# Optimization experiments

Measured on AMD Instinct MI355X. Metric: run time of the kernel, lower is better.

## Reference

```python
import jax, jax.numpy as jnp
import numpy as np

TOP_K = 8
TEMPERATURE = 0.07
EPS = 1e-12  # matches torch F.normalize eps


def l2norm(x):
    return x / jnp.maximum(jnp.linalg.norm(x, axis=-1, keepdims=True), EPS)


def setup_inputs() -> dict:
    key = jax.random.key(0)
    k1, k2, k3, k4 = jax.random.split(key, 4)
    B, D, V, U, Q = 256, 768, 50257, 1000, 10000
    time_series_embedding = jax.random.normal(k1, (B, D), dtype=jnp.float32)
    word_embeddings = jax.random.normal(k2, (V, D), dtype=jnp.float32)
    # xavier_uniform-like init scale for the prototype parameter
    limit = float(np.sqrt(6.0 / (U + D)))
    tctp_embeddings = jax.random.uniform(k3, (U, D), dtype=jnp.float32, minval=-limit, maxval=limit)
    support_set = jax.random.normal(k4, (Q, D), dtype=jnp.float32)
    return {
        "time_series_embedding": time_series_embedding,
        "word_embeddings": word_embeddings,
        "tctp_embeddings": tctp_embeddings,
        "support_set": support_set,
    }


def reference(time_series_embedding, word_embeddings, tctp_embeddings, support_set):
    B = time_series_embedding.shape[0]

    # ---- L_proto: MSE between each word token and its nearest prototype ----
    # For unit vectors, cdist^2 = 2 - 2*cos_sim, so argmin(dist) == argmax(sim).
    w_norm = l2norm(word_embeddings)          # [V, D]
    t_norm = l2norm(tctp_embeddings)          # [U, D]
    sim_vu = jnp.einsum('vd,ud->vu', w_norm, t_norm)  # [V, U]
    nearest_idx = jnp.argmax(sim_vu, axis=1)          # [V]
    nearest_protos = t_norm[nearest_idx]              # [V, D]
    loss_proto = jnp.mean((w_norm - nearest_protos) ** 2)

    # ---- top-k nearest-neighbor TCTPs from the support set ----
    ts_norm = l2norm(time_series_embedding)   # [B, D]
    sup_norm = l2norm(support_set)            # [Q, D]
    sim_bq = jnp.einsum('bd,qd->bq', ts_norm, sup_norm)  # [B, Q]
    # smallest L2 distance == largest cosine similarity (unit vectors)
    _, topk_idx = jax.lax.top_k(sim_bq, TOP_K)           # [B, k]
    nearest_tctps = sup_norm[topk_idx]                   # [B, k, D]

    # ---- NNCL contrastive loss ----
    positive = l2norm(nearest_tctps.mean(axis=1))        # [B, D]
    pos_sim = jnp.sum(ts_norm * positive, axis=1) / TEMPERATURE   # [B]
    neg_sim = jnp.einsum('bd,cd->bc', ts_norm, ts_norm) / TEMPERATURE  # [B, B]
    neg_sim = jnp.where(jnp.eye(B, dtype=bool), -jnp.inf, neg_sim)
    logits = jnp.concatenate([pos_sim[:, None], neg_sim], axis=1)  # [B, 1+B]
    loss_nncl = -jnp.mean(jax.nn.log_softmax(logits, axis=1)[:, 0])

    return nearest_tctps, loss_proto, loss_nncl
```

## Files before the change

### kernel.cpp

```cpp
#include <hip/hip_runtime.h>
#include <hip/hip_bf16.h>
#include <math.h>

typedef __bf16 bf16_t;
typedef __bf16 bf16x8 __attribute__((ext_vector_type(8)));
typedef __bf16 bf16x4 __attribute__((ext_vector_type(4)));
typedef float  f32x4  __attribute__((ext_vector_type(4)));
typedef long   i64_t;
typedef unsigned long long u64_t;

#define D 768

__device__ inline double blk_sum(double x, double* s) {
#pragma unroll
  for (int m = 32; m; m >>= 1) x += __shfl_xor(x, m);
  __syncthreads();
  if ((threadIdx.x & 63) == 0) s[threadIdx.x >> 6] = x;
  __syncthreads();
  return s[0] + s[1] + s[2] + s[3];
}

__device__ inline double blk_max(double x, double* s) {
#pragma unroll
  for (int m = 32; m; m >>= 1) x = fmax(x, __shfl_xor(x, m));
  __syncthreads();
  if ((threadIdx.x & 63) == 0) s[threadIdx.x >> 6] = x;
  __syncthreads();
  return fmax(fmax(s[0], s[1]), fmax(s[2], s[3]));
}

__global__ __launch_bounds__(256) void norm_all(
    const float* __restrict__ Tm, const float* __restrict__ TS,
    const float* __restrict__ SUP, const float* __restrict__ Wm,
    u64_t* __restrict__ t8T, u64_t* __restrict__ w8t,
    float* __restrict__ wscale, float* __restrict__ ts_n,
    bf16_t* __restrict__ ts_bf, float* __restrict__ sup_n,
    double* __restrict__ accd,
    int U, int V, int B, int Q, int nbT, int nbTS, int nbSUP) {
  const int wave = threadIdx.x >> 6, lane = threadIdx.x & 63;
  const int bid = blockIdx.x;
  if (bid == 0 && threadIdx.x == 0) accd[0] = 0.0;

  if (bid < nbT) {
    const int row = bid * 4 + wave;
    double inv = 0.0;
    if (row < U) {
      const float4* s = (const float4*)(Tm + (size_t)row * D);
      double ss = 0.0;
#pragma unroll
      for (int j = 0; j < 3; j++) {
        float4 v = s[lane + 64 * j];
        ss += (double)v.x * v.x + (double)v.y * v.y +
              (double)v.z * v.z + (double)v.w * v.w;
      }
#pragma unroll
      for (int m = 32; m; m >>= 1) ss += __shfl_xor(ss, m);
      inv = 1.0 / fmax(sqrt(ss), 1e-12);
    }
    const float sc = (float)(inv * 16.0);
#pragma unroll
    for (int h = 0; h < 2; h++) {
      if (h == 1 && lane >= 32) continue;
      const int c = h * 64 + lane;
      u64_t frag = 0ull;
      if (row < U) {
        const float* p = Tm + (size_t)row * D + c * 8;
        float4 x = *(const float4*)p;
        float4 y = *(const float4*)(p + 4);
        int lo = __builtin_amdgcn_cvt_pk_fp8_f32(x.x * sc, x.y * sc, 0, false);
        lo = __builtin_amdgcn_cvt_pk_fp8_f32(x.z * sc, x.w * sc, lo, true);
        int hi = __builtin_amdgcn_cvt_pk_fp8_f32(y.x * sc, y.y * sc, 0, false);
        hi = __builtin_amdgcn_cvt_pk_fp8_f32(y.z * sc, y.w * sc, hi, true);
        frag = ((u64_t)(unsigned)hi << 32) | (unsigned)lo;
      }
      t8T[(size_t)c * 1024 + row] = frag;
    }
    return;
  }

  if (bid < nbT + nbTS + nbSUP) {
    const float* src;
    int row;
    bool is_ts = false;
    if (bid < nbT + nbTS) { row = (bid - nbT) * 4 + wave; src = TS; is_ts = true; }
    else                  { row = (bid - nbT - nbTS) * 4 + wave; src = SUP;
                            if (row >= Q) return; }
    const float4* s = (const float4*)(src + (size_t)row * D);
    float4 v[3];
    double ss = 0.0;
#pragma unroll
    for (int j = 0; j < 3; j++) {
      v[j] = s[lane + 64 * j];
      ss += (double)v[j].x * v[j].x + (double)v[j].y * v[j].y +
            (double)v[j].z * v[j].z + (double)v[j].w * v[j].w;
    }
#pragma unroll
    for (int m = 32; m; m >>= 1) ss += __shfl_xor(ss, m);
    double inv = 1.0 / fmax(sqrt(ss), 1e-12);
    float4 o[3];
#pragma unroll
    for (int j = 0; j < 3; j++) {
      o[j].x = (float)((double)v[j].x * inv);
      o[j].y = (float)((double)v[j].y * inv);
      o[j].z = (float)((double)v[j].z * inv);
      o[j].w = (float)((double)v[j].w * inv);
    }
    float* dst = is_ts ? ts_n : sup_n;
    float* drow = dst + (size_t)row * D;
#pragma unroll
    for (int j = 0; j < 3; j++) ((float4*)drow)[lane + 64 * j] = o[j];
    if (is_ts) {
      bf16_t* brow = ts_bf + (size_t)row * D;
#pragma unroll
      for (int j = 0; j < 3; j++) {
        bf16x4 ob;
        ob[0] = (bf16_t)o[j].x; ob[1] = (bf16_t)o[j].y;
        ob[2] = (bf16_t)o[j].z; ob[3] = (bf16_t)o[j].w;
        *(bf16x4*)(brow + 4 * (lane + 64 * j)) = ob;
      }
    }
    return;
  }

  {
    const int v0 = (bid - nbT - nbTS - nbSUP) * 64 + wave * 16;
    const int r  = lane & 15;
    const int cs = lane >> 4;
    const int v  = v0 + r;
    const bool valid = v < V;
    const float* Wp = Wm + (size_t)v * D;
    u64_t* tile = w8t + (size_t)(v0 >> 4) * 1536;
    float ssf = 0.f;
#pragma unroll
    for (int j = 0; j < 24; j++) {
      u64_t frag = 0ull;
      if (valid) {
        const float* p = Wp + (j * 4 + cs) * 8;
        float4 x = *(const float4*)p;
        float4 y = *(const float4*)(p + 4);
        ssf += x.x * x.x + x.y * x.y + x.z * x.z + x.w * x.w +
               y.x * y.x + y.y * y.y + y.z * y.z + y.w * y.w;
        int lo = __builtin_amdgcn_cvt_pk_fp8_f32(x.x * 16.f, x.y * 16.f, 0, false);
        lo = __builtin_amdgcn_cvt_pk_fp8_f32(x.z * 16.f, x.w * 16.f, lo, true);
        int hi = __builtin_amdgcn_cvt_pk_fp8_f32(y.x * 16.f, y.y * 16.f, 0, false);
        hi = __builtin_amdgcn_cvt_pk_fp8_f32(y.z * 16.f, y.w * 16.f, hi, true);
        frag = ((u64_t)(unsigned)hi << 32) | (unsigned)lo;
      }
      tile[j * 64 + lane] = frag;
    }
    ssf += __shfl_xor(ssf, 16);
    ssf += __shfl_xor(ssf, 32);
    if (cs == 0)
      wscale[v0 + r] = valid
          ? (float)(1.0 / (256.0 * fmax(sqrt((double)ssf), 1e-12)))
          : 0.f;
  }
}

__global__ __launch_bounds__(256) void maxsim_gemm(
    const u64_t* __restrict__ W8T, const u64_t* __restrict__ T8T,
    float* __restrict__ maxpart, int U, int vstride) {
  __shared__ u64_t bt[4 * 96 * 16];
  const int tid  = threadIdx.x;
  const int lane = tid & 63;
  const int r    = lane & 15;
  const int ks   = lane >> 4;
  const int g    = blockIdx.x;

  {
    const int pb = g * 64;
#pragma unroll
    for (int j = 0; j < 12; j++) {
      const int m = j * 256 + tid;
      const int s = m / 768;
      const int rem = m - s * 768;
      const int c = rem >> 3, h = rem & 7;
      ulonglong2 val = *(const ulonglong2*)(T8T + (size_t)c * 1024 + pb + s * 16 + h * 2);
      *(ulonglong2*)(bt + s * 1536 + c * 16 + h * 2) = val;
    }
  }
  __syncthreads();

  bool msk[4];
#pragma unroll
  for (int s = 0; s < 4; s++) msk[s] = (g * 64 + s * 16 + r) < U;

  const int wv = tid >> 6;
#pragma unroll
  for (int wt = 0; wt < 4; wt++) {
    const int v0 = blockIdx.y * 256 + wv * 64 + wt * 16;
    const u64_t* ap = W8T + (size_t)(v0 >> 4) * 1536;
    u64_t a[24];
#pragma unroll
    for (int kk = 0; kk < 24; kk++) a[kk] = ap[kk * 64 + lane];
    f32x4 ac0 = {0.f,0.f,0.f,0.f}, ac1 = {0.f,0.f,0.f,0.f};
    f32x4 ac2 = {0.f,0.f,0.f,0.f}, ac3 = {0.f,0.f,0.f,0.f};
#pragma unroll
    for (int kk = 0; kk < 24; kk++) {
      const int ci = kk * 64 + lane;
      ac0 = __builtin_amdgcn_mfma_f32_16x16x32_fp8_fp8(
          (i64_t)a[kk], (i64_t)bt[ci],            ac0, 0, 0, 0);
      ac1 = __builtin_amdgcn_mfma_f32_16x16x32_fp8_fp8(
          (i64_t)a[kk], (i64_t)bt[1536 + ci],     ac1, 0, 0, 0);
      ac2 = __builtin_amdgcn_mfma_f32_16x16x32_fp8_fp8(
          (i64_t)a[kk], (i64_t)bt[2 * 1536 + ci], ac2, 0, 0, 0);
      ac3 = __builtin_amdgcn_mfma_f32_16x16x32_fp8_fp8(
          (i64_t)a[kk], (i64_t)bt[3 * 1536 + ci], ac3, 0, 0, 0);
    }
    f32x4 mx = {-1e30f, -1e30f, -1e30f, -1e30f};
#pragma unroll
    for (int j = 0; j < 4; j++) {
      if (msk[0]) mx[j] = fmaxf(mx[j], ac0[j]);
      if (msk[1]) mx[j] = fmaxf(mx[j], ac1[j]);
      if (msk[2]) mx[j] = fmaxf(mx[j], ac2[j]);
      if (msk[3]) mx[j] = fmaxf(mx[j], ac3[j]);
    }
#pragma unroll
    for (int m = 1; m < 16; m <<= 1) {
#pragma unroll
      for (int j = 0; j < 4; j++) mx[j] = fmaxf(mx[j], __shfl_xor(mx[j], m));
    }
    if (r == 0) {
#pragma unroll
      for (int j = 0; j < 4; j++)
        maxpart[(size_t)g * vstride + v0 + ks * 4 + j] = mx[j];
    }
  }
}

#define LDSROW 776

__global__ __launch_bounds__(256) void simf_gemm(const float* __restrict__ SUPn,
                                                 const bf16_t* __restrict__ TSb,
                                                 float* __restrict__ sim,
                                                 int Q, int ld, int NTB) {
  __shared__ __align__(16) bf16_t lds[2][16 * LDSROW];
  const int tid  = threadIdx.x;
  const int lane = tid & 63;
  const int rowbase = blockIdx.x * 64 + (tid >> 6) * 16;
  const int arow_i  = rowbase + (lane & 15);

  bf16x8 a[24];
  if (arow_i < Q) {
    const float* ar = SUPn + (size_t)arow_i * D + ((lane >> 4) * 8);
#pragma unroll
    for (int kk = 0; kk < 24; kk++) {
      float4 x = *(const float4*)(ar + kk * 32);
      float4 y = *(const float4*)(ar + kk * 32 + 4);
      bf16x8 f;
      f[0] = (bf16_t)x.x; f[1] = (bf16_t)x.y; f[2] = (bf16_t)x.z; f[3] = (bf16_t)x.w;
      f[4] = (bf16_t)y.x; f[5] = (bf16_t)y.y; f[6] = (bf16_t)y.z; f[7] = (bf16_t)y.w;
      a[kk] = f;
    }
  } else {
#pragma unroll
    for (int kk = 0; kk < 24; kk++) {
      bf16x8 f;
#pragma unroll
      for (int e = 0; e < 8; e++) f[e] = (bf16_t)0.f;
      a[kk] = f;
    }
  }

  auto stage = [&](int buf, int nt) {
    const ulonglong2* src = (const ulonglong2*)(TSb + (size_t)nt * 16 * D);
#pragma unroll
    for (int j = 0; j < 6; j++) {
      int c = tid + j * 256;
      int rr = c / 96, w = c % 96;
      *(ulonglong2*)&lds[buf][rr * LDSROW + w * 8] = src[c];
    }
  };

  stage(0, 0);
  for (int nt = 0; nt < NTB; nt++) {
    __syncthreads();
    if (nt + 1 < NTB) stage((nt + 1) & 1, nt + 1);
    f32x4 acc = {0.f, 0.f, 0.f, 0.f};
    const bf16_t* brow = &lds[nt & 1][(lane & 15) * LDSROW + ((lane >> 4) * 8)];
#pragma unroll
    for (int kk = 0; kk < 24; kk++) {
      bf16x8 b = *(const bf16x8*)(brow + kk * 32);
      acc = __builtin_amdgcn_mfma_f32_16x16x32_bf16(a[kk], b, acc, 0, 0, 0);
    }
    const int bcol = nt * 16 + (lane & 15);
    const int q0   = rowbase + ((lane >> 4) << 2);
    float* dst = sim + (size_t)bcol * ld + q0;
    if (q0 + 3 < Q) {
      *(f32x4*)dst = acc;
    } else {
#pragma unroll
      for (int j = 0; j < 4; j++)
        if (q0 + j < Q) dst[j] = acc[j];
    }
  }
}

__device__ inline unsigned long long pack_key(float v, int q) {
  unsigned u = __float_as_uint(v);
  u = (u & 0x80000000u) ? ~u : (u | 0x80000000u);
  return ((unsigned long long)u << 32) | (unsigned)(0xFFFFFFFFu - (unsigned)q);
}

__global__ __launch_bounds__(256) void topk_nncl(const float* __restrict__ sim,
                                                 const float* __restrict__ SUPn,
                                                 const float* __restrict__ TSn,
                                                 float* __restrict__ out,
                                                 double* __restrict__ row_loss,
                                                 int Q, int ld) {
  __shared__ unsigned long long sk[256][16];
  __shared__ float tsrow[D];
  __shared__ double sval[16];
  __shared__ int    sidx[16];
  __shared__ double red[4];
  const int b = blockIdx.x, tid = threadIdx.x;
#pragma unroll
  for (int j = 0; j < 3; j++) tsrow[tid + 256 * j] = TSn[(size_t)b * D + tid + 256 * j];

  const float* row = sim + (size_t)b * ld;
  unsigned long long best[16];
#pragma unroll
  for (int k = 0; k < 16; k++) best[k] = 0ull;
  for (int q = tid; q < Q; q += 256) {
    unsigned long long key = pack_key(row[q], q);
    if (key > best[15]) {
      best[15] = key;
      for (int k = 15; k > 0; k--) {
        if (best[k] > best[k - 1]) {
          unsigned long long t = best[k]; best[k] = best[k - 1]; best[k - 1] = t;
        } else break;
      }
    }
  }
#pragma unroll
  for (int k = 0; k < 16; k++) sk[tid][k] = best[k];
  for (int stride = 128; stride >= 1; stride >>= 1) {
    __syncthreads();
    if (tid < stride) {
      unsigned long long outk[16];
      int pa = 0, pb = 0;
#pragma unroll
      for (int k = 0; k < 16; k++) {
        unsigned long long va = sk[tid][pa], vb = sk[tid + stride][pb];
        if (va >= vb) { outk[k] = va; pa++; }
        else          { outk[k] = vb; pb++; }
      }
#pragma unroll
      for (int k = 0; k < 16; k++) sk[tid][k] = outk[k];
    }
  }
  __syncthreads();

  const int lane = tid & 63, w = tid >> 6;
  for (int c = w; c < 16; c += 4) {
    int q = (int)(0xFFFFFFFFu - (unsigned)(sk[0][c] & 0xFFFFFFFFull));
    const float* sr = SUPn + (size_t)q * D;
    double dot = 0.0;
#pragma unroll
    for (int i = 0; i < 12; i++)
      dot += (double)sr[lane + 64 * i] * (double)tsrow[lane + 64 * i];
#pragma unroll
    for (int m = 32; m; m >>= 1) dot += __shfl_xor(dot, m);
    if (lane == 0) { sval[c] = dot; sidx[c] = q; }
  }
  __syncthreads();
  if (tid == 0) {
    for (int i = 1; i < 16; i++) {
      double v = sval[i]; int ix = sidx[i];
      int j = i - 1;
      while (j >= 0 && (sval[j] < v || (sval[j] == v && sidx[j] > ix))) {
        sval[j + 1] = sval[j]; sidx[j + 1] = sidx[j]; j--;
      }
      sval[j + 1] = v; sidx[j + 1] = ix;
    }
  }
  __syncthreads();

  float mean[3] = {0.f, 0.f, 0.f};
#pragma unroll
  for (int k = 0; k < 8; k++) {
    const float* sr = SUPn + (size_t)sidx[k] * D;
    float* orow = out + ((size_t)b * 8 + k) * D;
#pragma unroll
    for (int j = 0; j < 3; j++) {
      float x = sr[tid + 256 * j];
      orow[tid + 256 * j] = x;
      mean[j] += x;
    }
  }
#pragma unroll
  for (int j = 0; j < 3; j++) mean[j] *= 0.125f;
  double ss = 0.0;
#pragma unroll
  for (int j = 0; j < 3; j++) ss += (double)mean[j] * mean[j];
  ss = blk_sum(ss, red);
  double inv = 1.0 / fmax(sqrt(ss), 1e-12);
  double dot = 0.0;
#pragma unroll
  for (int j = 0; j < 3; j++)
    dot += (double)tsrow[tid + 256 * j] * ((double)mean[j] * inv);
  dot = blk_sum(dot, red);
  const double p = dot / (double)0.07f;

  const float* tc = TSn + (size_t)tid * D;
  double dot2 = 0.0;
  for (int e = 0; e < D; e += 4) {
    float4 t4 = *(const float4*)(tc + e);
    dot2 += (double)tsrow[e] * t4.x + (double)tsrow[e + 1] * t4.y +
            (double)tsrow[e + 2] * t4.z + (double)tsrow[e + 3] * t4.w;
  }
  const bool diag = (tid == b);
  double logit = dot2 / (double)0.07f;
  double m = blk_max(diag ? -1e300 : logit, red);
  m = fmax(m, p);
  double term = diag ? 0.0 : exp(logit - m);
  double ssum = blk_sum(term, red);
  ssum += exp(p - m);
  if (tid == 0) row_loss[b] = (log(ssum) + m) - p;
}

__global__ __launch_bounds__(256) void reduce_proto(
    const float* __restrict__ maxpart, const float* __restrict__ wscale,
    double* __restrict__ accd, int V, int vstride) {
  __shared__ double red[4];
  const int v = blockIdx.x * 256 + threadIdx.x;
  double s = 0.0;
  if (v < V) {
    float mx = -1e30f;
#pragma unroll
    for (int g = 0; g < 16; g++)
      mx = fmaxf(mx, maxpart[(size_t)g * vstride + v]);
    s = 2.0 - 2.0 * (double)mx * (double)wscale[v];
  }
  s = blk_sum(s, red);
  if (threadIdx.x == 0) atomicAdd(accd, s);
}

__global__ __launch_bounds__(256) void finalize(const double* __restrict__ accd,
                                                const double* __restrict__ row_loss,
                                                float* __restrict__ d_out, int out_size,
                                                int V, int B) {
  __shared__ double red[4];
  const int tid = threadIdx.x;
  double s2 = 0.0;
  for (int b = tid; b < B; b += 256) s2 += row_loss[b];
  s2 = blk_sum(s2, red);
  if (tid == 0) {
    d_out[out_size - 2] = (float)(accd[0] / ((double)V * (double)D));
    d_out[out_size - 1] = (float)(s2 / (double)B);
  }
}

extern "C" void kernel_launch(void* const* d_in, const int* in_sizes, int n_in,
                              void* d_out, int out_size, void* d_ws, size_t ws_size,
                              hipStream_t stream) {
  const float* TS  = (const float*)d_in[0];
  const float* W   = (const float*)d_in[1];
  const float* T   = (const float*)d_in[2];
  const float* SUP = (const float*)d_in[3];
  const int B = in_sizes[0] / D;
  const int V = in_sizes[1] / D;
  const int U = in_sizes[2] / D;
  const int Q = in_sizes[3] / D;
  const int VPAD = (V + 255) & ~255;
  const int QPAD = (Q + 63) & ~63;
  const int NTB  = B / 16;
  const int nbT  = 1024 / 4;
  const int nbTS = B / 4;
  const int nbSUP = (Q + 3) / 4;
  const int nbW  = VPAD / 64;

  char* ws = (char*)d_ws;
  size_t off = 0;
  auto alloc = [&](size_t bytes) -> char* {
    char* p = ws + off;
    off = (off + bytes + 255) & ~(size_t)255;
    return p;
  };
  u64_t*  t8T    = (u64_t*) alloc((size_t)96 * 1024 * 8);
  u64_t*  w8t    = (u64_t*) alloc((size_t)(VPAD / 16) * 1536 * 8);
  float*  wscale = (float*) alloc((size_t)VPAD * 4);
  float*  maxpart= (float*) alloc((size_t)16 * VPAD * 4);
  float*  ts_n   = (float*) alloc((size_t)B * D * 4);
  bf16_t* ts_bf  = (bf16_t*)alloc((size_t)B * D * 2);
  float*  sup_n  = (float*) alloc((size_t)Q * D * 4);
  float*  simf   = (float*) alloc((size_t)B * QPAD * 4);
  double* rloss  = (double*)alloc((size_t)B * 8);
  double* accd   = (double*)alloc(8);
  (void)ws_size; (void)n_in;

  norm_all<<<nbT + nbTS + nbSUP + nbW, 256, 0, stream>>>(
      T, TS, SUP, W, t8T, w8t, wscale, ts_n, ts_bf, sup_n, accd,
      U, V, B, Q, nbT, nbTS, nbSUP);

  dim3 gms(16, VPAD / 256);
  maxsim_gemm<<<gms, 256, 0, stream>>>(w8t, t8T, maxpart, U, VPAD);

  simf_gemm<<<QPAD / 64, 256, 0, stream>>>(sup_n, ts_bf, simf, Q, QPAD, NTB);
  topk_nncl<<<B, 256, 0, stream>>>(simf, sup_n, ts_n, (float*)d_out, rloss, Q, QPAD);
  reduce_proto<<<VPAD / 256, 256, 0, stream>>>(maxpart, wscale, accd, V, VPAD);
  finalize<<<1, 256, 0, stream>>>(accd, rloss, (float*)d_out, out_size, V, B);
}
```

Before: 222.9 us.

## Split top-k into chunked partial pass and precompute gram matrix via tiled GEMM

The per-row top-k scan over the support similarities is split across four query chunks per batch row, with a small merge step in the NNCL kernel. This raises parallelism from one block per row. The B×B self-similarity is now computed by a separate shared-memory tiled fp32 GEMM instead of a per-thread fp64 dot loop, and the word-embedding fp8 conversion loop batches its loads before converting. This adds two kernel launches, and the gram logits lose fp64 accumulation precision.

```diff
diff --git a/kernel.cpp b/kernel.cpp
--- a/kernel.cpp
+++ b/kernel.cpp
@@ -130,23 +130,28 @@
     const bool valid = v < V;
     const float* Wp = Wm + (size_t)v * D;
     u64_t* tile = w8t + (size_t)(v0 >> 4) * 1536;
+    const float4 z4 = {0.f, 0.f, 0.f, 0.f};
     float ssf = 0.f;
 #pragma unroll
-    for (int j = 0; j < 24; j++) {
-      u64_t frag = 0ull;
-      if (valid) {
-        const float* p = Wp + (j * 4 + cs) * 8;
-        float4 x = *(const float4*)p;
-        float4 y = *(const float4*)(p + 4);
-        ssf += x.x * x.x + x.y * x.y + x.z * x.z + x.w * x.w +
-               y.x * y.x + y.y * y.y + y.z * y.z + y.w * y.w;
-        int lo = __builtin_amdgcn_cvt_pk_fp8_f32(x.x * 16.f, x.y * 16.f, 0, false);
-        lo = __builtin_amdgcn_cvt_pk_fp8_f32(x.z * 16.f, x.w * 16.f, lo, true);
-        int hi = __builtin_amdgcn_cvt_pk_fp8_f32(y.x * 16.f, y.y * 16.f, 0, false);
-        hi = __builtin_amdgcn_cvt_pk_fp8_f32(y.z * 16.f, y.w * 16.f, hi, true);
-        frag = ((u64_t)(unsigned)hi << 32) | (unsigned)lo;
-      }
-      tile[j * 64 + lane] = frag;
+    for (int jb = 0; jb < 6; jb++) {
+      float4 x[4], y[4];
+#pragma unroll
+      for (int u = 0; u < 4; u++) {
+        const float* p = Wp + ((jb * 4 + u) * 4 + cs) * 8;
+        x[u] = valid ? *(const float4*)p : z4;
+        y[u] = valid ? *(const float4*)(p + 4) : z4;
+      }
+#pragma unroll
+      for (int u = 0; u < 4; u++) {
+        ssf += x[u].x * x[u].x + x[u].y * x[u].y + x[u].z * x[u].z +
+               x[u].w * x[u].w + y[u].x * y[u].x + y[u].y * y[u].y +
+               y[u].z * y[u].z + y[u].w * y[u].w;
+        int lo = __builtin_amdgcn_cvt_pk_fp8_f32(x[u].x * 16.f, x[u].y * 16.f, 0, false);
+        lo = __builtin_amdgcn_cvt_pk_fp8_f32(x[u].z * 16.f, x[u].w * 16.f, lo, true);
+        int hi = __builtin_amdgcn_cvt_pk_fp8_f32(y[u].x * 16.f, y[u].y * 16.f, 0, false);
+        hi = __builtin_amdgcn_cvt_pk_fp8_f32(y[u].z * 16.f, y[u].w * 16.f, hi, true);
+        tile[(jb * 4 + u) * 64 + lane] = ((u64_t)(unsigned)hi << 32) | (unsigned)lo;
+      }
     }
     ssf += __shfl_xor(ssf, 16);
     ssf += __shfl_xor(ssf, 32);
@@ -296,32 +301,61 @@
   }
 }
 
+__global__ __launch_bounds__(256) void gram_gemm(const float* __restrict__ TSn,
+                                                 float* __restrict__ gram, int Bn) {
+  __shared__ float As[16][68];
+  __shared__ float Bs[16][68];
+  const int tid = threadIdx.x;
+  const int tx = tid & 15, ty = tid >> 4;
+  const int m0 = blockIdx.y * 64, n0 = blockIdx.x * 64;
+  const int sr = tid >> 2, sk = (tid & 3) * 4;
+  float acc[4][4] = {};
+  for (int k0 = 0; k0 < D; k0 += 16) {
+    __syncthreads();
+    float4 av = *(const float4*)(TSn + (size_t)(m0 + sr) * D + k0 + sk);
+    float4 bv = *(const float4*)(TSn + (size_t)(n0 + sr) * D + k0 + sk);
+    As[sk + 0][sr] = av.x; As[sk + 1][sr] = av.y;
+    As[sk + 2][sr] = av.z; As[sk + 3][sr] = av.w;
+    Bs[sk + 0][sr] = bv.x; Bs[sk + 1][sr] = bv.y;
+    Bs[sk + 2][sr] = bv.z; Bs[sk + 3][sr] = bv.w;
+    __syncthreads();
+#pragma unroll
+    for (int k = 0; k < 16; k++) {
+      float a0 = As[k][ty * 4 + 0], a1 = As[k][ty * 4 + 1];
+      float a2 = As[k][ty * 4 + 2], a3 = As[k][ty * 4 + 3];
+      float b0 = Bs[k][tx * 4 + 0], b1 = Bs[k][tx * 4 + 1];
+      float b2 = Bs[k][tx * 4 + 2], b3 = Bs[k][tx * 4 + 3];
+      acc[0][0] += a0 * b0; acc[0][1] += a0 * b1; acc[0][2] += a0 * b2; acc[0][3] += a0 * b3;
+      acc[1][0] += a1 * b0; acc[1][1] += a1 * b1; acc[1][2] += a1 * b2; acc[1][3] += a1 * b3;
+      acc[2][0] += a2 * b0; acc[2][1] += a2 * b1; acc[2][2] += a2 * b2; acc[2][3] += a2 * b3;
+      acc[3][0] += a3 * b0; acc[3][1] += a3 * b1; acc[3][2] += a3 * b2; acc[3][3] += a3 * b3;
+    }
+  }
+#pragma unroll
+  for (int i = 0; i < 4; i++) {
+    float4 o = {acc[i][0], acc[i][1], acc[i][2], acc[i][3]};
+    *(float4*)(gram + (size_t)(m0 + ty * 4 + i) * Bn + n0 + tx * 4) = o;
+  }
+}
+
 __device__ inline unsigned long long pack_key(float v, int q) {
   unsigned u = __float_as_uint(v);
   u = (u & 0x80000000u) ? ~u : (u | 0x80000000u);
   return ((unsigned long long)u << 32) | (unsigned)(0xFFFFFFFFu - (unsigned)q);
 }
 
-__global__ __launch_bounds__(256) void topk_nncl(const float* __restrict__ sim,
-                                                 const float* __restrict__ SUPn,
-                                                 const float* __restrict__ TSn,
-                                                 float* __restrict__ out,
-                                                 double* __restrict__ row_loss,
-                                                 int Q, int ld) {
+__global__ __launch_bounds__(256) void topk_part(const float* __restrict__ sim,
+                                                 u64_t* __restrict__ cand_keys,
+                                                 int Q, int ld, int qc) {
   __shared__ unsigned long long sk[256][16];
-  __shared__ float tsrow[D];
-  __shared__ double sval[16];
-  __shared__ int    sidx[16];
-  __shared__ double red[4];
-  const int b = blockIdx.x, tid = threadIdx.x;
-#pragma unroll
-  for (int j = 0; j < 3; j++) tsrow[tid + 256 * j] = TSn[(size_t)b * D + tid + 256 * j];
-
+  const int b = blockIdx.y, chunk = blockIdx.x, tid = threadIdx.x;
   const float* row = sim + (size_t)b * ld;
+  const int q0 = chunk * qc;
+  const int q1 = min(Q, q0 + qc);
   unsigned long long best[16];
 #pragma unroll
   for (int k = 0; k < 16; k++) best[k] = 0ull;
-  for (int q = tid; q < Q; q += 256) {
+  for (int q = q0 + tid; q < q1; q += 256) {
     unsigned long long key = pack_key(row[q], q);
     if (key > best[15]) {
       best[15] = key;
@@ -350,10 +384,45 @@
     }
   }
   __syncthreads();
+  if (tid < 16) cand_keys[((size_t)b * 4 + chunk) * 16 + tid] = sk[0][tid];
+}
+
+__global__ __launch_bounds__(256) void topk_nncl(const u64_t* __restrict__ cand_keys,
+                                                 const float* __restrict__ gram,
+                                                 const float* __restrict__ SUPn,
+                                                 const float* __restrict__ TSn,
+                                                 float* __restrict__ out,
+                                                 double* __restrict__ row_loss,
+                                                 int Bn) {
+  __shared__ u64_t keys[64];
+  __shared__ u64_t merged[16];
+  __shared__ float tsrow[D];
+  __shared__ double sval[16];
+  __shared__ int    sidx[16];
+  __shared__ double red[4];
+  const int b = blockIdx.x, tid = threadIdx.x;
+#pragma unroll
+  for (int j = 0; j < 3; j++) tsrow[tid + 256 * j] = TSn[(size_t)b * D + tid + 256 * j];
+  if (tid < 64) keys[tid] = cand_keys[(size_t)b * 64 + tid];
+  __syncthreads();
+  if (tid == 0) {
+    int p[4] = {0, 0, 0, 0};
+    for (int k = 0; k < 16; k++) {
+      u64_t bestv = 0ull; int bi = 0;
+#pragma unroll
+      for (int c = 0; c < 4; c++) {
+        u64_t v = (p[c] < 16) ? keys[c * 16 + p[c]] : 0ull;
+        if (v > bestv) { bestv = v; bi = c; }
+      }
+      merged[k] = bestv;
+      p[bi]++;
+    }
+  }
+  __syncthreads();
 
   const int lane = tid & 63, w = tid >> 6;
   for (int c = w; c < 16; c += 4) {
-    int q = (int)(0xFFFFFFFFu - (unsigned)(sk[0][c] & 0xFFFFFFFFull));
+    int q = (int)(0xFFFFFFFFu - (unsigned)(merged[c] & 0xFFFFFFFFull));
     const float* sr = SUPn + (size_t)q * D;
     double dot = 0.0;
 #pragma unroll
@@ -402,15 +471,8 @@
   dot = blk_sum(dot, red);
   const double p = dot / (double)0.07f;
 
-  const float* tc = TSn + (size_t)tid * D;
-  double dot2 = 0.0;
-  for (int e = 0; e < D; e += 4) {
-    float4 t4 = *(const float4*)(tc + e);
-    dot2 += (double)tsrow[e] * t4.x + (double)tsrow[e + 1] * t4.y +
-            (double)tsrow[e + 2] * t4.z + (double)tsrow[e + 3] * t4.w;
-  }
   const bool diag = (tid == b);
-  double logit = dot2 / (double)0.07f;
+  double logit = (double)gram[(size_t)b * Bn + tid] / (double)0.07f;
   double m = blk_max(diag ? -1e300 : logit, red);
   m = fmax(m, p);
   double term = diag ? 0.0 : exp(logit - m);
@@ -469,6 +531,7 @@
   const int nbTS = B / 4;
   const int nbSUP = (Q + 3) / 4;
   const int nbW  = VPAD / 64;
+  const int QC   = QPAD / 4;
 
   char* ws = (char*)d_ws;
   size_t off = 0;
@@ -485,6 +548,8 @@
   bf16_t* ts_bf  = (bf16_t*)alloc((size_t)B * D * 2);
   float*  sup_n  = (float*) alloc((size_t)Q * D * 4);
   float*  simf   = (float*) alloc((size_t)B * QPAD * 4);
+  float*  gram   = (float*) alloc((size_t)B * B * 4);
+  u64_t*  ckeys  = (u64_t*) alloc((size_t)B * 64 * 8);
   double* rloss  = (double*)alloc((size_t)B * 8);
   double* accd   = (double*)alloc(8);
   (void)ws_size; (void)n_in;
@@ -497,7 +562,14 @@
   maxsim_gemm<<<gms, 256, 0, stream>>>(w8t, t8T, maxpart, U, VPAD);
 
   simf_gemm<<<QPAD / 64, 256, 0, stream>>>(sup_n, ts_bf, simf, Q, QPAD, NTB);
-  topk_nncl<<<B, 256, 0, stream>>>(simf, sup_n, ts_n, (float*)d_out, rloss, Q, QPAD);
+
+  dim3 ggr(B / 64, B / 64);
+  gram_gemm<<<ggr, 256, 0, stream>>>(ts_n, gram, B);
+
+  dim3 gtp(4, B);
+  topk_part<<<gtp, 256, 0, stream>>>(simf, ckeys, Q, QPAD, QC);
+
+  topk_nncl<<<B, 256, 0, stream>>>(ckeys, gram, sup_n, ts_n, (float*)d_out, rloss, B);
   reduce_proto<<<VPAD / 256, 256, 0, stream>>>(maxpart, wscale, accd, V, VPAD);
   finalize<<<1, 256, 0, stream>>>(accd, rloss, (float*)d_out, out_size, V, B);
 }
```

New measurement: 278.1 us. 1.25x slower.

## Move word-embedding FP8 quantization into the top-k kernel to overlap work

Applied to the files above, without the earlier changes.

The word-embedding normalize/FP8-quantize work moves out of the first normalization kernel and into a combined launch alongside the per-row top-k/NNCL blocks. The small normalize kernel and the support-set GEMM now run first, and the launch order is rearranged. The aim is to fill the GPU with the bandwidth-heavy W quantization while the 256 top-k blocks, which would otherwise underuse the device, are running. In exchange, the top-k work now waits on the GEMM before any W quantization starts, and maxsim_gemm still depends on the combined kernel.

```diff
diff --git a/kernel.cpp b/kernel.cpp
--- a/kernel.cpp
+++ b/kernel.cpp
@@ -29,14 +29,12 @@
   return fmax(fmax(s[0], s[1]), fmax(s[2], s[3]));
 }
 
-__global__ __launch_bounds__(256) void norm_all(
+__global__ __launch_bounds__(256) void norm_rest(
     const float* __restrict__ Tm, const float* __restrict__ TS,
-    const float* __restrict__ SUP, const float* __restrict__ Wm,
-    u64_t* __restrict__ t8T, u64_t* __restrict__ w8t,
-    float* __restrict__ wscale, float* __restrict__ ts_n,
-    bf16_t* __restrict__ ts_bf, float* __restrict__ sup_n,
-    double* __restrict__ accd,
-    int U, int V, int B, int Q, int nbT, int nbTS, int nbSUP) {
+    const float* __restrict__ SUP, u64_t* __restrict__ t8T,
+    float* __restrict__ ts_n, bf16_t* __restrict__ ts_bf,
+    float* __restrict__ sup_n, double* __restrict__ accd,
+    int U, int B, int Q, int nbT, int nbTS) {
   const int wave = threadIdx.x >> 6, lane = threadIdx.x & 63;
   const int bid = blockIdx.x;
   if (bid == 0 && threadIdx.x == 0) accd[0] = 0.0;
@@ -78,52 +76,138 @@
     return;
   }
 
-  if (bid < nbT + nbTS + nbSUP) {
-    const float* src;
-    int row;
-    bool is_ts = false;
-    if (bid < nbT + nbTS) { row = (bid - nbT) * 4 + wave; src = TS; is_ts = true; }
-    else                  { row = (bid - nbT - nbTS) * 4 + wave; src = SUP;
-                            if (row >= Q) return; }
-    const float4* s = (const float4*)(src + (size_t)row * D);
-    float4 v[3];
-    double ss = 0.0;
+  const float* src;
+  int row;
+  bool is_ts = false;
+  if (bid < nbT + nbTS) { row = (bid - nbT) * 4 + wave; src = TS; is_ts = true; }
+  else                  { row = (bid - nbT - nbTS) * 4 + wave; src = SUP;
+                          if (row >= Q) return; }
+  const float4* s = (const float4*)(src + (size_t)row * D);
+  float4 v[3];
+  double ss = 0.0;
+#pragma unroll
+  for (int j = 0; j < 3; j++) {
+    v[j] = s[lane + 64 * j];
+    ss += (double)v[j].x * v[j].x + (double)v[j].y * v[j].y +
+          (double)v[j].z * v[j].z + (double)v[j].w * v[j].w;
+  }
+#pragma unroll
+  for (int m = 32; m; m >>= 1) ss += __shfl_xor(ss, m);
+  double inv = 1.0 / fmax(sqrt(ss), 1e-12);
+  float4 o[3];
+#pragma unroll
+  for (int j = 0; j < 3; j++) {
+    o[j].x = (float)((double)v[j].x * inv);
+    o[j].y = (float)((double)v[j].y * inv);
+    o[j].z = (float)((double)v[j].z * inv);
+    o[j].w = (float)((double)v[j].w * inv);
+  }
+  float* dst = is_ts ? ts_n : sup_n;
+  float* drow = dst + (size_t)row * D;
+#pragma unroll
+  for (int j = 0; j < 3; j++) ((float4*)drow)[lane + 64 * j] = o[j];
+  if (is_ts) {
+    bf16_t* brow = ts_bf + (size_t)row * D;
 #pragma unroll
     for (int j = 0; j < 3; j++) {
-      v[j] = s[lane + 64 * j];
-      ss += (double)v[j].x * v[j].x + (double)v[j].y * v[j].y +
-            (double)v[j].z * v[j].z + (double)v[j].w * v[j].w;
-    }
-#pragma unroll
-    for (int m = 32; m; m >>= 1) ss += __shfl_xor(ss, m);
-    double inv = 1.0 / fmax(sqrt(ss), 1e-12);
-    float4 o[3];
-#pragma unroll
-    for (int j = 0; j < 3; j++) {
-      o[j].x = (float)((double)v[j].x * inv);
-      o[j].y = (float)((double)v[j].y * inv);
-      o[j].z = (float)((double)v[j].z * inv);
-      o[j].w = (float)((double)v[j].w * inv);
-    }
-    float* dst = is_ts ? ts_n : sup_n;
-    float* drow = dst + (size_t)row * D;
-#pragma unroll
-    for (int j = 0; j < 3; j++) ((float4*)drow)[lane + 64 * j] = o[j];
-    if (is_ts) {
-      bf16_t* brow = ts_bf + (size_t)row * D;
-#pragma unroll
-      for (int j = 0; j < 3; j++) {
-        bf16x4 ob;
-        ob[0] = (bf16_t)o[j].x; ob[1] = (bf16_t)o[j].y;
-        ob[2] = (bf16_t)o[j].z; ob[3] = (bf16_t)o[j].w;
-        *(bf16x4*)(brow + 4 * (lane + 64 * j)) = ob;
-      }
-    }
-    return;
-  }
-
-  {
-    const int v0 = (bid - nbT - nbTS - nbSUP) * 64 + wave * 16;
+      bf16x4 ob;
+      ob[0] = (bf16_t)o[j].x; ob[1] = (bf16_t)o[j].y;
+      ob[2] = (bf16_t)o[j].z; ob[3] = (bf16_t)o[j].w;
+      *(bf16x4*)(brow + 4 * (lane + 64 * j)) = ob;
+    }
+  }
+}
+
+#define LDSROW 776
+
+__global__ __launch_bounds__(256) void simf_gemm(const float* __restrict__ SUPn,
+                                                 const bf16_t* __restrict__ TSb,
+                                                 float* __restrict__ sim,
+                                                 int Q, int ld, int NTB) {
+  __shared__ __align__(16) bf16_t lds[2][16 * LDSROW];
+  const int tid  = threadIdx.x;
+  const int lane = tid & 63;
+  const int rowbase = blockIdx.x * 64 + (tid >> 6) * 16;
+  const int arow_i  = rowbase + (lane & 15);
+
+  bf16x8 a[24];
+  if (arow_i < Q) {
+    const float* ar = SUPn + (size_t)arow_i * D + ((lane >> 4) * 8);
+#pragma unroll
+    for (int kk = 0; kk < 24; kk++) {
+      float4 x = *(const float4*)(ar + kk * 32);
+      float4 y = *(const float4*)(ar + kk * 32 + 4);
+      bf16x8 f;
+      f[0] = (bf16_t)x.x; f[1] = (bf16_t)x.y; f[2] = (bf16_t)x.z; f[3] = (bf16_t)x.w;
+      f[4] = (bf16_t)y.x; f[5] = (bf16_t)y.y; f[6] = (bf16_t)y.z; f[7] = (bf16_t)y.w;
+      a[kk] = f;
+    }
+  } else {
+#pragma unroll
+    for (int kk = 0; kk < 24; kk++) {
+      bf16x8 f;
+#pragma unroll
+      for (int e = 0; e < 8; e++) f[e] = (bf16_t)0.f;
+      a[kk] = f;
+    }
+  }
+
+  auto stage = [&](int buf, int nt) {
+    const ulonglong2* src = (const ulonglong2*)(TSb + (size_t)nt * 16 * D);
+#pragma unroll
+    for (int j = 0; j < 6; j++) {
+      int c = tid + j * 256;
+      int rr = c / 96, w = c % 96;
+      *(ulonglong2*)&lds[buf][rr * LDSROW + w * 8] = src[c];
+    }
+  };
+
+  stage(0, 0);
+  for (int nt = 0; nt < NTB; nt++) {
+    __syncthreads();
+    if (nt + 1 < NTB) stage((nt + 1) & 1, nt + 1);
+    f32x4 acc = {0.f, 0.f, 0.f, 0.f};
+    const bf16_t* brow = &lds[nt & 1][(lane & 15) * LDSROW + ((lane >> 4) * 8)];
+#pragma unroll
+    for (int kk = 0; kk < 24; kk++) {
+      bf16x8 b = *(const bf16x8*)(brow + kk * 32);
+      acc = __builtin_amdgcn_mfma_f32_16x16x32_bf16(a[kk], b, acc, 0, 0, 0);
+    }
+    const int bcol = nt * 16 + (lane & 15);
+    const int q0   = rowbase + ((lane >> 4) << 2);
+    float* dst = sim + (size_t)bcol * ld + q0;
+    if (q0 + 3 < Q) {
+      *(f32x4*)dst = acc;
+    } else {
+#pragma unroll
+      for (int j = 0; j < 4; j++)
+        if (q0 + j < Q) dst[j] = acc[j];
+    }
+  }
+}
+
+__device__ inline unsigned long long pack_key(float v, int q) {
+  unsigned u = __float_as_uint(v);
+  u = (u & 0x80000000u) ? ~u : (u | 0x80000000u);
+  return ((unsigned long long)u << 32) | (unsigned)(0xFFFFFFFFu - (unsigned)q);
+}
+
+__global__ __launch_bounds__(256) void fused_topk_wquant(
+    const float* __restrict__ sim, const float* __restrict__ SUPn,
+    const float* __restrict__ TSn, const float* __restrict__ Wm,
+    u64_t* __restrict__ w8t, float* __restrict__ wscale,
+    float* __restrict__ out, double* __restrict__ row_loss,
+    int Q, int ld, int V, int nbTopk) {
+  __shared__ unsigned long long sk[256][16];
+  __shared__ float tsrow[D];
+  __shared__ double sval[16];
+  __shared__ int    sidx[16];
+  __shared__ double red[4];
+  const int tid = threadIdx.x;
+
+  if (blockIdx.x >= nbTopk) {
+    const int wave = tid >> 6, lane = tid & 63;
+    const int v0 = (blockIdx.x - nbTopk) * 64 + wave * 16;
     const int r  = lane & 15;
     const int cs = lane >> 4;
     const int v  = v0 + r;
@@ -154,7 +238,113 @@
       wscale[v0 + r] = valid
           ? (float)(1.0 / (256.0 * fmax(sqrt((double)ssf), 1e-12)))
           : 0.f;
-  }
+    return;
+  }
+
+  const int b = blockIdx.x;
+#pragma unroll
+  for (int j = 0; j < 3; j++) tsrow[tid + 256 * j] = TSn[(size_t)b * D + tid + 256 * j];
+
+  const float* row = sim + (size_t)b * ld;
+  unsigned long long best[16];
+#pragma unroll
+  for (int k = 0; k < 16; k++) best[k] = 0ull;
+  for (int q = tid; q < Q; q += 256) {
+    unsigned long long key = pack_key(row[q], q);
+    if (key > best[15]) {
+      best[15] = key;
+      for (int k = 15; k > 0; k--) {
+        if (best[k] > best[k - 1]) {
+          unsigned long long t = best[k]; best[k] = best[k - 1]; best[k - 1] = t;
+        } else break;
+      }
+    }
+  }
+#pragma unroll
+  for (int k = 0; k < 16; k++) sk[tid][k] = best[k];
+  for (int stride = 128; stride >= 1; stride >>= 1) {
+    __syncthreads();
+    if (tid < stride) {
+      unsigned long long outk[16];
+      int pa = 0, pb = 0;
+#pragma unroll
+      for (int k = 0; k < 16; k++) {
+        unsigned long long va = sk[tid][pa], vb = sk[tid + stride][pb];
+        if (va >= vb) { outk[k] = va; pa++; }
+        else          { outk[k] = vb; pb++; }
+      }
+#pragma unroll
+      for (int k = 0; k < 16; k++) sk[tid][k] = outk[k];
+    }
+  }
+  __syncthreads();
+
+  const int lane = tid & 63, w = tid >> 6;
+  for (int c = w; c < 16; c += 4) {
+    int q = (int)(0xFFFFFFFFu - (unsigned)(sk[0][c] & 0xFFFFFFFFull));
+    const float* sr = SUPn + (size_t)q * D;
+    double dot = 0.0;
+#pragma unroll
+    for (int i = 0; i < 12; i++)
+      dot += (double)sr[lane + 64 * i] * (double)tsrow[lane + 64 * i];
+#pragma unroll
+    for (int m = 32; m; m >>= 1) dot += __shfl_xor(dot, m);
+    if (lane == 0) { sval[c] = dot; sidx[c] = q; }
+  }
+  __syncthreads();
+  if (tid == 0) {
+    for (int i = 1; i < 16; i++) {
+      double v = sval[i]; int ix = sidx[i];
+      int j = i - 1;
+      while (j >= 0 && (sval[j] < v || (sval[j] == v && sidx[j] > ix))) {
+        sval[j + 1] = sval[j]; sidx[j + 1] = sidx[j]; j--;
+      }
+      sval[j + 1] = v; sidx[j + 1] = ix;
+    }
+  }
+  __syncthreads();
+
+  float mean[3] = {0.f, 0.f, 0.f};
+#pragma unroll
+  for (int k = 0; k < 8; k++) {
+    const float* sr = SUPn + (size_t)sidx[k] * D;
+    float* orow = out + ((size_t)b * 8 + k) * D;
+#pragma unroll
+    for (int j = 0; j < 3; j++) {
+      float x = sr[tid + 256 * j];
+      orow[tid + 256 * j] = x;
+      mean[j] += x;
+    }
+  }
+#pragma unroll
+  for (int j = 0; j < 3; j++) mean[j] *= 0.125f;
+  double ss = 0.0;
+#pragma unroll
+  for (int j = 0; j < 3; j++) ss += (double)mean[j] * mean[j];
+  ss = blk_sum(ss, red);
+  double inv = 1.0 / fmax(sqrt(ss), 1e-12);
+  double dot = 0.0;
+#pragma unroll
+  for (int j = 0; j < 3; j++)
+    dot += (double)tsrow[tid + 256 * j] * ((double)mean[j] * inv);
+  dot = blk_sum(dot, red);
+  const double p = dot / (double)0.07f;
+
+  const float* tc = TSn + (size_t)tid * D;
+  double dot2 = 0.0;
+  for (int e = 0; e < D; e += 4) {
+    float4 t4 = *(const float4*)(tc + e);
+    dot2 += (double)tsrow[e] * t4.x + (double)tsrow[e + 1] * t4.y +
+            (double)tsrow[e + 2] * t4.z + (double)tsrow[e + 3] * t4.w;
+  }
+  const bool diag = (tid == b);
+  double logit = dot2 / (double)0.07f;
+  double m = blk_max(diag ? -1e300 : logit, red);
+  m = fmax(m, p);
+  double term = diag ? 0.0 : exp(logit - m);
+  double ssum = blk_sum(term, red);
+  ssum += exp(p - m);
+  if (tid == 0) row_loss[b] = (log(ssum) + m) - p;
 }
 
 __global__ __launch_bounds__(256) void maxsim_gemm(
@@ -226,197 +416,6 @@
         maxpart[(size_t)g * vstride + v0 + ks * 4 + j] = mx[j];
     }
   }
-}
-
-#define LDSROW 776
-
-__global__ __launch_bounds__(256) void simf_gemm(const float* __restrict__ SUPn,
-                                                 const bf16_t* __restrict__ TSb,
-                                                 float* __restrict__ sim,
-                                                 int Q, int ld, int NTB) {
-  __shared__ __align__(16) bf16_t lds[2][16 * LDSROW];
-  const int tid  = threadIdx.x;
-  const int lane = tid & 63;
-  const int rowbase = blockIdx.x * 64 + (tid >> 6) * 16;
-  const int arow_i  = rowbase + (lane & 15);
-
-  bf16x8 a[24];
-  if (arow_i < Q) {
-    const float* ar = SUPn + (size_t)arow_i * D + ((lane >> 4) * 8);
-#pragma unroll
-    for (int kk = 0; kk < 24; kk++) {
-      float4 x = *(const float4*)(ar + kk * 32);
-      float4 y = *(const float4*)(ar + kk * 32 + 4);
-      bf16x8 f;
-      f[0] = (bf16_t)x.x; f[1] = (bf16_t)x.y; f[2] = (bf16_t)x.z; f[3] = (bf16_t)x.w;
-      f[4] = (bf16_t)y.x; f[5] = (bf16_t)y.y; f[6] = (bf16_t)y.z; f[7] = (bf16_t)y.w;
-      a[kk] = f;
-    }
-  } else {
-#pragma unroll
-    for (int kk = 0; kk < 24; kk++) {
-      bf16x8 f;
-#pragma unroll
-      for (int e = 0; e < 8; e++) f[e] = (bf16_t)0.f;
-      a[kk] = f;
-    }
-  }
-
-  auto stage = [&](int buf, int nt) {
-    const ulonglong2* src = (const ulonglong2*)(TSb + (size_t)nt * 16 * D);
-#pragma unroll
-    for (int j = 0; j < 6; j++) {
-      int c = tid + j * 256;
-      int rr = c / 96, w = c % 96;
-      *(ulonglong2*)&lds[buf][rr * LDSROW + w * 8] = src[c];
-    }
-  };
-
-  stage(0, 0);
-  for (int nt = 0; nt < NTB; nt++) {
-    __syncthreads();
-    if (nt + 1 < NTB) stage((nt + 1) & 1, nt + 1);
-    f32x4 acc = {0.f, 0.f, 0.f, 0.f};
-    const bf16_t* brow = &lds[nt & 1][(lane & 15) * LDSROW + ((lane >> 4) * 8)];
-#pragma unroll
-    for (int kk = 0; kk < 24; kk++) {
-      bf16x8 b = *(const bf16x8*)(brow + kk * 32);
-      acc = __builtin_amdgcn_mfma_f32_16x16x32_bf16(a[kk], b, acc, 0, 0, 0);
-    }
-    const int bcol = nt * 16 + (lane & 15);
-    const int q0   = rowbase + ((lane >> 4) << 2);
-    float* dst = sim + (size_t)bcol * ld + q0;
-    if (q0 + 3 < Q) {
-      *(f32x4*)dst = acc;
-    } else {
-#pragma unroll
-      for (int j = 0; j < 4; j++)
-        if (q0 + j < Q) dst[j] = acc[j];
-    }
-  }
-}
-
-__device__ inline unsigned long long pack_key(float v, int q) {
-  unsigned u = __float_as_uint(v);
-  u = (u & 0x80000000u) ? ~u : (u | 0x80000000u);
-  return ((unsigned long long)u << 32) | (unsigned)(0xFFFFFFFFu - (unsigned)q);
-}
-
-__global__ __launch_bounds__(256) void topk_nncl(const float* __restrict__ sim,
-                                                 const float* __restrict__ SUPn,
-                                                 const float* __restrict__ TSn,
-                                                 float* __restrict__ out,
-                                                 double* __restrict__ row_loss,
-                                                 int Q, int ld) {
-  __shared__ unsigned long long sk[256][16];
-  __shared__ float tsrow[D];
-  __shared__ double sval[16];
-  __shared__ int    sidx[16];
-  __shared__ double red[4];
-  const int b = blockIdx.x, tid = threadIdx.x;
-#pragma unroll
-  for (int j = 0; j < 3; j++) tsrow[tid + 256 * j] = TSn[(size_t)b * D + tid + 256 * j];
-
-  const float* row = sim + (size_t)b * ld;
-  unsigned long long best[16];
-#pragma unroll
-  for (int k = 0; k < 16; k++) best[k] = 0ull;
-  for (int q = tid; q < Q; q += 256) {
-    unsigned long long key = pack_key(row[q], q);
-    if (key > best[15]) {
-      best[15] = key;
-      for (int k = 15; k > 0; k--) {
-        if (best[k] > best[k - 1]) {
-          unsigned long long t = best[k]; best[k] = best[k - 1]; best[k - 1] = t;
-        } else break;
-      }
-    }
-  }
-#pragma unroll
-  for (int k = 0; k < 16; k++) sk[tid][k] = best[k];
-  for (int stride = 128; stride >= 1; stride >>= 1) {
-    __syncthreads();
-    if (tid < stride) {
-      unsigned long long outk[16];
-      int pa = 0, pb = 0;
-#pragma unroll
-      for (int k = 0; k < 16; k++) {
-        unsigned long long va = sk[tid][pa], vb = sk[tid + stride][pb];
-        if (va >= vb) { outk[k] = va; pa++; }
-        else          { outk[k] = vb; pb++; }
-      }
-#pragma unroll
-      for (int k = 0; k < 16; k++) sk[tid][k] = outk[k];
-    }
-  }
-  __syncthreads();
-
-  const int lane = tid & 63, w = tid >> 6;
-  for (int c = w; c < 16; c += 4) {
-    int q = (int)(0xFFFFFFFFu - (unsigned)(sk[0][c] & 0xFFFFFFFFull));
-    const float* sr = SUPn + (size_t)q * D;
-    double dot = 0.0;
-#pragma unroll
-    for (int i = 0; i < 12; i++)
-      dot += (double)sr[lane + 64 * i] * (double)tsrow[lane + 64 * i];
-#pragma unroll
-    for (int m = 32; m; m >>= 1) dot += __shfl_xor(dot, m);
-    if (lane == 0) { sval[c] = dot; sidx[c] = q; }
-  }
-  __syncthreads();
-  if (tid == 0) {
-    for (int i = 1; i < 16; i++) {
-      double v = sval[i]; int ix = sidx[i];
-      int j = i - 1;
-      while (j >= 0 && (sval[j] < v || (sval[j] == v && sidx[j] > ix))) {
-        sval[j + 1] = sval[j]; sidx[j + 1] = sidx[j]; j--;
-      }
-      sval[j + 1] = v; sidx[j + 1] = ix;
-    }
-  }
-  __syncthreads();
-
-  float mean[3] = {0.f, 0.f, 0.f};
-#pragma unroll
-  for (int k = 0; k < 8; k++) {
-    const float* sr = SUPn + (size_t)sidx[k] * D;
-    float* orow = out + ((size_t)b * 8 + k) * D;
-#pragma unroll
-    for (int j = 0; j < 3; j++) {
-      float x = sr[tid + 256 * j];
-      orow[tid + 256 * j] = x;
-      mean[j] += x;
-    }
-  }
-#pragma unroll
-  for (int j = 0; j < 3; j++) mean[j] *= 0.125f;
-  double ss = 0.0;
-#pragma unroll
-  for (int j = 0; j < 3; j++) ss += (double)mean[j] * mean[j];
-  ss = blk_sum(ss, red);
-  double inv = 1.0 / fmax(sqrt(ss), 1e-12);
-  double dot = 0.0;
-#pragma unroll
-  for (int j = 0; j < 3; j++)
-    dot += (double)tsrow[tid + 256 * j] * ((double)mean[j] * inv);
-  dot = blk_sum(dot, red);
-  const double p = dot / (double)0.07f;
-
-  const float* tc = TSn + (size_t)tid * D;
-  double dot2 = 0.0;
-  for (int e = 0; e < D; e += 4) {
-    float4 t4 = *(const float4*)(tc + e);
-    dot2 += (double)tsrow[e] * t4.x + (double)tsrow[e + 1] * t4.y +
-            (double)tsrow[e + 2] * t4.z + (double)tsrow[e + 3] * t4.w;
-  }
-  const bool diag = (tid == b);
-  double logit = dot2 / (double)0.07f;
-  double m = blk_max(diag ? -1e300 : logit, red);
-  m = fmax(m, p);
-  double term = diag ? 0.0 : exp(logit - m);
-  double ssum = blk_sum(term, red);
-  ssum += exp(p - m);
-  if (tid == 0) row_loss[b] = (log(ssum) + m) - p;
 }
 
 __global__ __launch_bounds__(256) void reduce_proto(
@@ -465,10 +464,10 @@
   const int VPAD = (V + 255) & ~255;
   const int QPAD = (Q + 63) & ~63;
   const int NTB  = B / 16;
+  const int nbW  = VPAD / 64;
   const int nbT  = 1024 / 4;
   const int nbTS = B / 4;
   const int nbSUP = (Q + 3) / 4;
-  const int nbW  = VPAD / 64;
 
   char* ws = (char*)d_ws;
   size_t off = 0;
@@ -489,15 +488,17 @@
   double* accd   = (double*)alloc(8);
   (void)ws_size; (void)n_in;
 
-  norm_all<<<nbT + nbTS + nbSUP + nbW, 256, 0, stream>>>(
-      T, TS, SUP, W, t8T, w8t, wscale, ts_n, ts_bf, sup_n, accd,
-      U, V, B, Q, nbT, nbTS, nbSUP);
+  norm_rest<<<nbT + nbTS + nbSUP, 256, 0, stream>>>(
+      T, TS, SUP, t8T, ts_n, ts_bf, sup_n, accd, U, B, Q, nbT, nbTS);
+
+  simf_gemm<<<QPAD / 64, 256, 0, stream>>>(sup_n, ts_bf, simf, Q, QPAD, NTB);
+
+  fused_topk_wquant<<<B + nbW, 256, 0, stream>>>(
+      simf, sup_n, ts_n, W, w8t, wscale, (float*)d_out, rloss, Q, QPAD, V, B);
 
   dim3 gms(16, VPAD / 256);
   maxsim_gemm<<<gms, 256, 0, stream>>>(w8t, t8T, maxpart, U, VPAD);
 
-  simf_gemm<<<QPAD / 64, 256, 0, stream>>>(sup_n, ts_bf, simf, Q, QPAD, NTB);
-  topk_nncl<<<B, 256, 0, stream>>>(simf, sup_n, ts_n, (float*)d_out, rloss, Q, QPAD);
   reduce_proto<<<VPAD / 256, 256, 0, stream>>>(maxpart, wscale, accd, V, VPAD);
   finalize<<<1, 256, 0, stream>>>(accd, rloss, (float*)d_out, out_size, V, B);
 }
```

Result: faster. 195.1 us, median of 2 (-12.5%).
